# Optimization experiments

Hardware: AMD Instinct MI355X
Metric: run time of the kernel (lower is better)

Reference implementation:

```python
import jax, jax.numpy as jnp
import numpy as np

N_PAPER, N_MESH = 60000, 30000
N = N_PAPER + N_MESH
E_TRAIN, E_DEC = 2000000, 400000
F_PAPER = F_MESH = 128
D0, H, D = 16, 32, 16  # initial embed, hidden, final embed
NREL, NB = 2, 4


def _glorot(key, shape):
    fan_in, fan_out = shape[-2], shape[-1]
    s = jnp.sqrt(6.0 / (fan_in + fan_out)).astype(jnp.float32)
    return jax.random.uniform(key, shape, jnp.float32, -s, s)


def setup_inputs() -> dict:
    key = jax.random.key(0)
    ks = iter(jax.random.split(key, 40))
    inp = {
        'x_paper': jax.random.normal(next(ks), (N_PAPER, F_PAPER), jnp.float32),
        'x_mesh': jax.random.normal(next(ks), (N_MESH, F_MESH), jnp.float32),
        'train_edge_index': jax.random.randint(next(ks), (2, E_TRAIN), 0, N, jnp.int64 if jax.config.jax_enable_x64 else jnp.int32),
        'train_edge_type': jnp.sort(jax.random.randint(next(ks), (E_TRAIN,), 0, NREL)),
        'pos_edge_index': jax.random.randint(next(ks), (2, E_DEC), 0, N),
        'pos_edge_type': jnp.sort(jax.random.randint(next(ks), (E_DEC,), 0, NREL)),
        'neg_edge_index': jax.random.randint(next(ks), (2, E_DEC), 0, N),
        'neg_edge_type': jnp.sort(jax.random.randint(next(ks), (E_DEC,), 0, NREL)),
        # input transforms
        'Wp': _glorot(next(ks), (F_PAPER, D0)), 'bp': jnp.zeros((D0,), jnp.float32),
        'Wm': _glorot(next(ks), (F_MESH, D0)), 'bm': jnp.zeros((D0,), jnp.float32),
        # decode linears
        'Wd0': _glorot(next(ks), (D, D)), 'bd0': jnp.zeros((D,), jnp.float32),
        'Wd1': _glorot(next(ks), (D, D)), 'bd1': jnp.zeros((D,), jnp.float32),
    }
    dims = [(D0, H), (H, H), (H, H), (H, D)]
    for i, (di, do) in enumerate(dims, 1):
        inp[f'bases{i}'] = _glorot(next(ks), (NB, di, do))
        inp[f'comp{i}'] = _glorot(next(ks), (NREL, NB))
        inp[f'root{i}'] = _glorot(next(ks), (di, do))
        inp[f'bias{i}'] = jnp.zeros((do,), jnp.float32)
    return inp


def rgcn_layer(x, src, dst, et, bases, comp, root, bias):
    # PyG RGCNConv with basis decomposition, per-relation mean aggregation.
    out = x @ root + bias
    xs = x[src]  # [E, in]
    for r in range(NREL):
        W_r = jnp.einsum('b,bio->io', comp[r], bases)
        m = xs @ W_r  # [E, out]
        mf = (et == r).astype(m.dtype)
        cnt = jax.ops.segment_sum(mf, dst, num_segments=N)
        agg = jax.ops.segment_sum(m * mf[:, None], dst, num_segments=N)
        out = out + agg / jnp.clip(cnt, 1.0)[:, None]
    return out


def _decode_block(z, ei, et, Wd0, bd0, Wd1, bd1):
    zs, zd = z[ei[0]], z[ei[1]]
    h0 = zs @ Wd0 + bd0
    h1 = zs @ Wd1 + bd1
    h = jnp.where((et == 0)[:, None], h0, h1)
    return jnp.sum(h * zd, axis=-1)


def reference(x_paper, x_mesh, train_edge_index, train_edge_type,
              pos_edge_index, pos_edge_type, neg_edge_index, neg_edge_type,
              Wp, bp, Wm, bm, Wd0, bd0, Wd1, bd1,
              bases1, comp1, root1, bias1, bases2, comp2, root2, bias2,
              bases3, comp3, root3, bias3, bases4, comp4, root4, bias4):
    x = jnp.concatenate([x_paper @ Wp + bp, x_mesh @ Wm + bm], axis=0)  # [N, D0]
    src, dst = train_edge_index[0], train_edge_index[1]
    x = jax.nn.relu(rgcn_layer(x, src, dst, train_edge_type, bases1, comp1, root1, bias1))
    x = jax.nn.relu(rgcn_layer(x, src, dst, train_edge_type, bases2, comp2, root2, bias2))
    x = jax.nn.relu(rgcn_layer(x, src, dst, train_edge_type, bases3, comp3, root3, bias3))
    z = rgcn_layer(x, src, dst, train_edge_type, bases4, comp4, root4, bias4)
    # edge types are sorted, so per-edge in-order compute matches the masked concat order
    pos = _decode_block(z, pos_edge_index, pos_edge_type, Wd0, bd0, Wd1, bd1)
    neg = _decode_block(z, neg_edge_index, neg_edge_type, Wd0, bd0, Wd1, bd1)
    return jnp.concatenate([pos, neg], axis=0)  # [2*E_DEC]
```

## Files before the change

kernel.cpp:

```cpp
#include <hip/hip_runtime.h>
#include <hip/hip_bf16.h>

constexpr int NN = 90000;
constexpr int NP = 60000;
constexpr int NM = 30000;
constexpr int ET = 2000000;
constexpr int ED = 400000;
constexpr int TWO_NN = 2 * NN;

constexpr int BKT_SH  = 9;
constexpr int NB_BKT  = (TWO_NN + 511) >> BKT_SH;
constexpr int BKT_CAP = 6400;
constexpr int TILE    = 2048;
constexpr int N_TILES = (ET + TILE - 1) / TILE;

__device__ __forceinline__ float bflo(unsigned int u) {
    union { unsigned int i; float f; } c;
    c.i = u << 16;
    return c.f;
}
__device__ __forceinline__ float bfhi(unsigned int u) {
    union { unsigned int i; float f; } c;
    c.i = u & 0xffff0000u;
    return c.f;
}
__device__ __forceinline__ unsigned short f2bf(float f) {
    union { float f; unsigned int i; } c;
    c.f = f;
    unsigned int x = c.i;
    return (unsigned short)((x + 0x7FFFu + ((x >> 16) & 1u)) >> 16);
}

__global__ void init_kernel(const int* __restrict__ tei, int* __restrict__ gcur,
                            int* __restrict__ dflag) {
    int b = blockIdx.x * blockDim.x + threadIdx.x;
    if (b < NB_BKT) gcur[b] = b * BKT_CAP;
    if (b == 0) {
        int allzero = 1;
        for (int i = 0; i < 16; i++)
            if (tei[2 * i + 1] != 0) allzero = 0;
        dflag[0] = allzero;
    }
}

__global__ void __launch_bounds__(256) binA_kernel(
        const int* __restrict__ ei, const int* __restrict__ et,
        const int* __restrict__ dflag, int* __restrict__ gcur,
        int2* __restrict__ pairs) {
    __shared__ int histw[4][NB_BKT];
    __shared__ int wbase[4][NB_BKT];
    __shared__ int tot[NB_BKT];
    __shared__ int excl[NB_BKT];
    __shared__ int gbase[NB_BKT];
    __shared__ int scn[256];
    __shared__ int2 tbuf[TILE];
    int t = threadIdx.x;
    int w = t >> 6;
    int tile0 = blockIdx.x * TILE;
    int tcount = ET - tile0;
    if (tcount > TILE) tcount = TILE;
    for (int i = t; i < 4 * NB_BKT; i += 256) ((int*)histw)[i] = 0;
    __syncthreads();
    int sft = dflag[0];
    int myk[8], mys[8];
#pragma unroll
    for (int q = 0; q < 8; q++) {
        int li = q * 256 + t;
        myk[q] = -1;
        if (li < tcount) {
            int e = tile0 + li;
            int s = ei[(size_t)e << sft];
            int d = ei[(size_t)(ET + e) << sft];
            int r = et[(size_t)e << sft];
            int key = r * NN + d;
            myk[q] = key;
            mys[q] = s;
            atomicAdd(&histw[w][key >> BKT_SH], 1);
        }
    }
    __syncthreads();
    for (int i = t; i < NB_BKT; i += 256) {
        int h0 = histw[0][i], h1 = histw[1][i], h2 = histw[2][i], h3 = histw[3][i];
        wbase[0][i] = 0;
        wbase[1][i] = h0;
        wbase[2][i] = h0 + h1;
        wbase[3][i] = h0 + h1 + h2;
        tot[i] = h0 + h1 + h2 + h3;
    }
    __syncthreads();
    int v0 = (t < NB_BKT / 2) ? tot[2 * t] : 0;
    int v1 = (t < NB_BKT / 2) ? tot[2 * t + 1] : 0;
    int s = v0 + v1;
    scn[t] = s;
    __syncthreads();
    for (int st = 1; st < 256; st <<= 1) {
        int u = (t >= st) ? scn[t - st] : 0;
        __syncthreads();
        scn[t] += u;
        __syncthreads();
    }
    int base = scn[t] - s;
    if (t < NB_BKT / 2) {
        excl[2 * t] = base;
        excl[2 * t + 1] = base + v0;
    }
    __syncthreads();
    for (int i = t; i < NB_BKT; i += 256) {
        int e0 = excl[i];
        wbase[0][i] += e0;
        wbase[1][i] += e0;
        wbase[2][i] += e0;
        wbase[3][i] += e0;
        histw[0][i] = 0; histw[1][i] = 0; histw[2][i] = 0; histw[3][i] = 0;
    }
    __syncthreads();
#pragma unroll
    for (int q = 0; q < 8; q++) {
        if (myk[q] >= 0) {
            int b = myk[q] >> BKT_SH;
            int p = wbase[w][b] + atomicAdd(&histw[w][b], 1);
            tbuf[p] = make_int2(myk[q], mys[q]);
        }
    }
    __syncthreads();
    for (int i = t; i < NB_BKT; i += 256)
        if (tot[i] > 0) gbase[i] = atomicAdd(&gcur[i], tot[i]);
    __syncthreads();
    for (int i = t; i < tcount; i += 256) {
        int2 p = tbuf[i];
        int b = p.x >> BKT_SH;
        int gpos = gbase[b] + (i - excl[b]);
        int cap = (b + 1) * BKT_CAP - 1;
        pairs[gpos < cap ? gpos : cap] = p;
    }
}

__global__ void __launch_bounds__(256) histplace_kernel(
        const int* __restrict__ gcur, const int2* __restrict__ pairs,
        int* __restrict__ off, int* __restrict__ endo, float* __restrict__ inv,
        int* __restrict__ csr) {
    __shared__ int kh[512];
    __shared__ int scn[256];
    int b = blockIdx.x;
    int t = threadIdx.x;
    int beg = b * BKT_CAP, end = gcur[b];
    for (int i = t; i < 512; i += 256) kh[i] = 0;
    __syncthreads();
    for (int i = beg + t; i < end; i += 256)
        atomicAdd(&kh[pairs[i].x & 511], 1);
    __syncthreads();
    int v[2];
    int s = 0;
#pragma unroll
    for (int q = 0; q < 2; q++) {
        v[q] = kh[t * 2 + q];
        s += v[q];
    }
    scn[t] = s;
    __syncthreads();
    for (int st = 1; st < 256; st <<= 1) {
        int u = (t >= st) ? scn[t - st] : 0;
        __syncthreads();
        scn[t] += u;
        __syncthreads();
    }
    int run = beg + scn[t] - s;
    int kbase = b << BKT_SH;
    int kc[2];
#pragma unroll
    for (int q = 0; q < 2; q++) {
        int key = kbase + t * 2 + q;
        if (key < TWO_NN) {
            off[key] = run;
            endo[key] = run + v[q];
            inv[key] = 1.0f / (float)(v[q] > 1 ? v[q] : 1);
        }
        kc[q] = run;
        run += v[q];
    }
    __syncthreads();
#pragma unroll
    for (int q = 0; q < 2; q++) kh[t * 2 + q] = kc[q];
    __syncthreads();
    for (int i = beg + t; i < end; i += 256) {
        int2 p = pairs[i];
        int pos = atomicAdd(&kh[p.x & 511], 1);
        csr[pos] = p.y;
    }
}

__global__ void __launch_bounds__(256) embed2_kernel(
        const float* __restrict__ Xp, const float* __restrict__ Xm,
        const float* __restrict__ Wp, const float* __restrict__ bp,
        const float* __restrict__ Wm, const float* __restrict__ bm,
        unsigned short* __restrict__ outbf) {
    __shared__ float Wl[4096 + 32];
    for (int i = threadIdx.x; i < 2048; i += 256) {
        Wl[i] = Wp[i];
        Wl[2048 + i] = Wm[i];
    }
    if (threadIdx.x < 16) {
        Wl[4096 + threadIdx.x] = bp[threadIdx.x];
        Wl[4112 + threadIdx.x] = bm[threadIdx.x];
    }
    __syncthreads();
    int n = blockIdx.x * 256 + threadIdx.x;
    if (n >= NN) return;
    const float* X;
    const float* Ws;
    const float* Bs;
    if (n < NP) { X = Xp + (size_t)n * 128; Ws = Wl; Bs = Wl + 4096; }
    else        { X = Xm + (size_t)(n - NP) * 128; Ws = Wl + 2048; Bs = Wl + 4112; }
    float acc[16];
#pragma unroll
    for (int j = 0; j < 16; j++) acc[j] = Bs[j];
    const float4* row = (const float4*)X;
    for (int k4 = 0; k4 < 32; k4++) {
        float4 xv = row[k4];
        int k = k4 * 4;
#pragma unroll
        for (int j = 0; j < 16; j++) {
            float a = acc[j];
            a = fmaf(xv.x, Ws[(k + 0) * 16 + j], a);
            a = fmaf(xv.y, Ws[(k + 1) * 16 + j], a);
            a = fmaf(xv.z, Ws[(k + 2) * 16 + j], a);
            a = fmaf(xv.w, Ws[(k + 3) * 16 + j], a);
            acc[j] = a;
        }
    }
    ushort4* ob = (ushort4*)(outbf + (size_t)n * 16);
#pragma unroll
    for (int q = 0; q < 4; q++) {
        ushort4 ub;
        ub.x = f2bf(acc[4 * q]);     ub.y = f2bf(acc[4 * q + 1]);
        ub.z = f2bf(acc[4 * q + 2]); ub.w = f2bf(acc[4 * q + 3]);
        ob[q] = ub;
    }
}

__global__ void prep_all_kernel(
        const float* __restrict__ ba0, const float* __restrict__ co0,
        const float* __restrict__ ro0, const float* __restrict__ bi0,
        const float* __restrict__ ba1, const float* __restrict__ co1,
        const float* __restrict__ ro1, const float* __restrict__ bi1,
        const float* __restrict__ ba2, const float* __restrict__ co2,
        const float* __restrict__ ro2, const float* __restrict__ bi2,
        const float* __restrict__ ba3, const float* __restrict__ co3,
        const float* __restrict__ ro3, const float* __restrict__ bi3,
        float* __restrict__ Wbuf4) {
    int l = blockIdx.x;
    const float* bases; const float* comp; const float* root; const float* bias;
    if (l == 0)      { bases = ba0; comp = co0; root = ro0; bias = bi0; }
    else if (l == 1) { bases = ba1; comp = co1; root = ro1; bias = bi1; }
    else if (l == 2) { bases = ba2; comp = co2; root = ro2; bias = bi2; }
    else             { bases = ba3; comp = co3; root = ro3; bias = bi3; }
    int din = (l == 0) ? 16 : 32;
    int dout = (l == 3) ? 16 : 32;
    int sz = din * dout;
    float* W = Wbuf4 + l * 3200;
    for (int i = threadIdx.x; i < sz; i += 256) {
        float b0 = bases[i];
        float b1 = bases[sz + i];
        float b2 = bases[2 * sz + i];
        float b3 = bases[3 * sz + i];
        for (int r = 0; r < 2; r++) {
            W[r * sz + i] = comp[r * 4 + 0] * b0 + comp[r * 4 + 1] * b1 +
                            comp[r * 4 + 2] * b2 + comp[r * 4 + 3] * b3;
        }
        W[2 * sz + i] = root[i];
    }
    if (threadIdx.x < dout) W[3 * sz + threadIdx.x] = bias[threadIdx.x];
}

template <int DIN, int DOUT, int RELU>
__global__ void __launch_bounds__(256) layer_kernel(
        const int* __restrict__ off, const int* __restrict__ endo,
        const int* __restrict__ csr,
        const unsigned short* __restrict__ xbf_in,
        const float* __restrict__ inv, const float* __restrict__ Wbuf,
        unsigned short* __restrict__ xbf_out) {
    constexpr int SZ = DIN * DOUT;
    constexpr int QL = DIN / 8;
    constexpr int TPN = 2 * QL;
    constexpr int NPB = 256 / TPN;
    constexpr int AGST = 2 * DIN + 4;
    constexpr int XSST = DIN + 8;
    __shared__ float Wl[3 * SZ + DOUT];
    __shared__ float agg[NPB * AGST];
    __shared__ unsigned short xsu[NPB * XSST];
    for (int i = threadIdx.x; i < 3 * SZ + DOUT; i += 256) Wl[i] = Wbuf[i];
    int t = threadIdx.x;
    int ln = t / TPN;
    int rl = t % TPN;
    int r = rl / QL;
    int lane = rl % QL;
    int d = blockIdx.x * NPB + ln;
    if (d < NN) {
        if (r == 0) {
            uint4 u = *(const uint4*)(xbf_in + (size_t)d * DIN + lane * 8);
            *(uint4*)&xsu[ln * XSST + lane * 8] = u;
        }
        int key = r * NN + d;
        int b = off[key];
        int e = endo[key];
        float a0[8] = {0, 0, 0, 0, 0, 0, 0, 0};
        float a1[8] = {0, 0, 0, 0, 0, 0, 0, 0};
        const unsigned short* hp = xbf_in + lane * 8;
        int k = b;
        if (k + 3 < e) {
            int s0 = csr[k], s1 = csr[k + 1], s2 = csr[k + 2], s3 = csr[k + 3];
            k += 4;
            while (k + 3 < e) {
                uint4 u0 = *(const uint4*)(hp + (size_t)s0 * DIN);
                uint4 u1 = *(const uint4*)(hp + (size_t)s1 * DIN);
                uint4 u2 = *(const uint4*)(hp + (size_t)s2 * DIN);
                uint4 u3 = *(const uint4*)(hp + (size_t)s3 * DIN);
                s0 = csr[k]; s1 = csr[k + 1]; s2 = csr[k + 2]; s3 = csr[k + 3];
                k += 4;
                a0[0] += bflo(u0.x); a0[1] += bfhi(u0.x);
                a0[2] += bflo(u0.y); a0[3] += bfhi(u0.y);
                a0[4] += bflo(u0.z); a0[5] += bfhi(u0.z);
                a0[6] += bflo(u0.w); a0[7] += bfhi(u0.w);
                a1[0] += bflo(u1.x); a1[1] += bfhi(u1.x);
                a1[2] += bflo(u1.y); a1[3] += bfhi(u1.y);
                a1[4] += bflo(u1.z); a1[5] += bfhi(u1.z);
                a1[6] += bflo(u1.w); a1[7] += bfhi(u1.w);
                a0[0] += bflo(u2.x); a0[1] += bfhi(u2.x);
                a0[2] += bflo(u2.y); a0[3] += bfhi(u2.y);
                a0[4] += bflo(u2.z); a0[5] += bfhi(u2.z);
                a0[6] += bflo(u2.w); a0[7] += bfhi(u2.w);
                a1[0] += bflo(u3.x); a1[1] += bfhi(u3.x);
                a1[2] += bflo(u3.y); a1[3] += bfhi(u3.y);
                a1[4] += bflo(u3.z); a1[5] += bfhi(u3.z);
                a1[6] += bflo(u3.w); a1[7] += bfhi(u3.w);
            }
            uint4 u0 = *(const uint4*)(hp + (size_t)s0 * DIN);
            uint4 u1 = *(const uint4*)(hp + (size_t)s1 * DIN);
            uint4 u2 = *(const uint4*)(hp + (size_t)s2 * DIN);
            uint4 u3 = *(const uint4*)(hp + (size_t)s3 * DIN);
            a0[0] += bflo(u0.x); a0[1] += bfhi(u0.x);
            a0[2] += bflo(u0.y); a0[3] += bfhi(u0.y);
            a0[4] += bflo(u0.z); a0[5] += bfhi(u0.z);
            a0[6] += bflo(u0.w); a0[7] += bfhi(u0.w);
            a1[0] += bflo(u1.x); a1[1] += bfhi(u1.x);
            a1[2] += bflo(u1.y); a1[3] += bfhi(u1.y);
            a1[4] += bflo(u1.z); a1[5] += bfhi(u1.z);
            a1[6] += bflo(u1.w); a1[7] += bfhi(u1.w);
            a0[0] += bflo(u2.x); a0[1] += bfhi(u2.x);
            a0[2] += bflo(u2.y); a0[3] += bfhi(u2.y);
            a0[4] += bflo(u2.z); a0[5] += bfhi(u2.z);
            a0[6] += bflo(u2.w); a0[7] += bfhi(u2.w);
            a1[0] += bflo(u3.x); a1[1] += bfhi(u3.x);
            a1[2] += bflo(u3.y); a1[3] += bfhi(u3.y);
            a1[4] += bflo(u3.z); a1[5] += bfhi(u3.z);
            a1[6] += bflo(u3.w); a1[7] += bfhi(u3.w);
        }
        for (; k < e; k++) {
            uint4 u0 = *(const uint4*)(hp + (size_t)csr[k] * DIN);
            a0[0] += bflo(u0.x); a0[1] += bfhi(u0.x);
            a0[2] += bflo(u0.y); a0[3] += bfhi(u0.y);
            a0[4] += bflo(u0.z); a0[5] += bfhi(u0.z);
            a0[6] += bflo(u0.w); a0[7] += bfhi(u0.w);
        }
        float* ap = agg + ln * AGST + r * DIN + lane * 8;
        *(float4*)ap = make_float4(a0[0] + a1[0], a0[1] + a1[1],
                                   a0[2] + a1[2], a0[3] + a1[3]);
        *(float4*)(ap + 4) = make_float4(a0[4] + a1[4], a0[5] + a1[5],
                                         a0[6] + a1[6], a0[7] + a1[7]);
    }
    __syncthreads();
    constexpr int CPN = DOUT / 4;
    for (int tt = t; tt < NPB * CPN; tt += 256) {
        int ln2 = tt / CPN;
        int j0 = (tt % CPN) * 4;
        int d2 = blockIdx.x * NPB + ln2;
        if (d2 < NN) {
            float iv0 = inv[d2], iv1 = inv[NN + d2];
            float acc[4];
#pragma unroll
            for (int jj = 0; jj < 4; jj++) acc[jj] = Wl[3 * SZ + j0 + jj];
#pragma unroll
            for (int k2 = 0; k2 < DIN; k2 += 2) {
                unsigned up = *(const unsigned*)&xsu[ln2 * XSST + k2];
                float xv0 = bflo(up);
                float xv1 = bfhi(up);
                float m00 = agg[ln2 * AGST + k2] * iv0;
                float m10 = agg[ln2 * AGST + DIN + k2] * iv1;
                float m01 = agg[ln2 * AGST + k2 + 1] * iv0;
                float m11 = agg[ln2 * AGST + DIN + k2 + 1] * iv1;
                const float* w0a = &Wl[k2 * DOUT + j0];
                const float* w1a = &Wl[SZ + k2 * DOUT + j0];
                const float* wra = &Wl[2 * SZ + k2 * DOUT + j0];
#pragma unroll
                for (int jj = 0; jj < 4; jj++) {
                    acc[jj] = fmaf(xv0, wra[jj], acc[jj]);
                    acc[jj] = fmaf(m00, w0a[jj], acc[jj]);
                    acc[jj] = fmaf(m10, w1a[jj], acc[jj]);
                    acc[jj] = fmaf(xv1, wra[DOUT + jj], acc[jj]);
                    acc[jj] = fmaf(m01, w0a[DOUT + jj], acc[jj]);
                    acc[jj] = fmaf(m11, w1a[DOUT + jj], acc[jj]);
                }
            }
            if (RELU) {
#pragma unroll
                for (int jj = 0; jj < 4; jj++) acc[jj] = fmaxf(acc[jj], 0.0f);
            }
            ushort4 ub;
            ub.x = f2bf(acc[0]); ub.y = f2bf(acc[1]);
            ub.z = f2bf(acc[2]); ub.w = f2bf(acc[3]);
            *(ushort4*)(xbf_out + (size_t)d2 * DOUT + j0) = ub;
        }
    }
}

__global__ void __launch_bounds__(256) decode_fused_kernel(
        const unsigned short* __restrict__ zbf,
        const float* __restrict__ Wd0, const float* __restrict__ bd0,
        const float* __restrict__ Wd1, const float* __restrict__ bd1,
        const int* __restrict__ pei, const int* __restrict__ pet,
        const int* __restrict__ nei, const int* __restrict__ net_,
        float* __restrict__ out, const int* __restrict__ dflag) {
    __shared__ float W[2][256];
    __shared__ float B[2][16];
    for (int i = threadIdx.x; i < 256; i += 256) {
        W[0][i] = Wd0[i];
        W[1][i] = Wd1[i];
    }
    if (threadIdx.x < 16) {
        B[0][threadIdx.x] = bd0[threadIdx.x];
        B[1][threadIdx.x] = bd1[threadIdx.x];
    }
    __syncthreads();
    int i = blockIdx.x * 256 + threadIdx.x;
    if (i >= 2 * ED) return;
    int sft = dflag[0];
    const int* ei;
    const int* et;
    int e;
    if (i < ED) { ei = pei; et = pet; e = i; }
    else        { ei = nei; et = net_; e = i - ED; }
    int s = ei[(size_t)e << sft];
    int d = ei[(size_t)(ED + e) << sft];
    int r = et[(size_t)e << sft];
    float zs[16], zd[16];
    const uint4* sp = (const uint4*)(zbf + ((size_t)s << 4));
    const uint4* dp = (const uint4*)(zbf + ((size_t)d << 4));
#pragma unroll
    for (int h = 0; h < 2; h++) {
        uint4 us = sp[h];
        uint4 ud = dp[h];
        int o8 = h * 8;
        zs[o8 + 0] = bflo(us.x); zs[o8 + 1] = bfhi(us.x);
        zs[o8 + 2] = bflo(us.y); zs[o8 + 3] = bfhi(us.y);
        zs[o8 + 4] = bflo(us.z); zs[o8 + 5] = bfhi(us.z);
        zs[o8 + 6] = bflo(us.w); zs[o8 + 7] = bfhi(us.w);
        zd[o8 + 0] = bflo(ud.x); zd[o8 + 1] = bfhi(ud.x);
        zd[o8 + 2] = bflo(ud.y); zd[o8 + 3] = bfhi(ud.y);
        zd[o8 + 4] = bflo(ud.z); zd[o8 + 5] = bfhi(ud.z);
        zd[o8 + 6] = bflo(ud.w); zd[o8 + 7] = bfhi(ud.w);
    }
    const float* Wr = W[r];
    const float* Br = B[r];
    float acc = 0.0f;
#pragma unroll
    for (int j = 0; j < 16; j++) {
        float yj = Br[j];
#pragma unroll
        for (int k = 0; k < 16; k++) yj = fmaf(zs[k], Wr[k * 16 + j], yj);
        acc = fmaf(yj, zd[j], acc);
    }
    out[i] = acc;
}

extern "C" void kernel_launch(void* const* d_in, const int* in_sizes, int n_in,
                              void* d_out, int out_size, void* d_ws, size_t ws_size,
                              hipStream_t stream) {
    const float* x_paper = (const float*)d_in[0];
    const float* x_mesh  = (const float*)d_in[1];
    const int* tei  = (const int*)d_in[2];
    const int* tet  = (const int*)d_in[3];
    const int* pei  = (const int*)d_in[4];
    const int* pet  = (const int*)d_in[5];
    const int* nei  = (const int*)d_in[6];
    const int* net_ = (const int*)d_in[7];
    const float* Wp  = (const float*)d_in[8];
    const float* bp  = (const float*)d_in[9];
    const float* Wm  = (const float*)d_in[10];
    const float* bm  = (const float*)d_in[11];
    const float* Wd0 = (const float*)d_in[12];
    const float* bd0 = (const float*)d_in[13];
    const float* Wd1 = (const float*)d_in[14];
    const float* bd1 = (const float*)d_in[15];

    float* ws = (float*)d_ws;
    size_t o = 0;
    unsigned short* xbfA = (unsigned short*)(ws + o); o += (size_t)NN * 16;
    unsigned short* xbfB = (unsigned short*)(ws + o); o += (size_t)NN * 16;
    float* inv  = ws + o; o += (size_t)TWO_NN;
    int*   off  = (int*)(ws + o); o += (size_t)TWO_NN;
    int*   endo = (int*)(ws + o); o += (size_t)TWO_NN;
    int*   csr  = (int*)(ws + o); o += (size_t)NB_BKT * BKT_CAP;
    int*   gcur = (int*)(ws + o); o += 512;
    int2*  pairs = (int2*)(ws + o); o += (size_t)2 * NB_BKT * BKT_CAP;
    float* Wbuf4 = ws + o; o += 4 * 3200;
    int*   dflag = (int*)(ws + o); o += 16;

    init_kernel<<<(NB_BKT + 255) / 256, 256, 0, stream>>>(tei, gcur, dflag);

    binA_kernel<<<N_TILES, 256, 0, stream>>>(tei, tet, dflag, gcur, pairs);
    histplace_kernel<<<NB_BKT, 256, 0, stream>>>(gcur, pairs, off, endo, inv, csr);

    embed2_kernel<<<(NN + 255) / 256, 256, 0, stream>>>(
        x_paper, x_mesh, Wp, bp, Wm, bm, xbfA);

    prep_all_kernel<<<4, 256, 0, stream>>>(
        (const float*)d_in[16], (const float*)d_in[17], (const float*)d_in[18], (const float*)d_in[19],
        (const float*)d_in[20], (const float*)d_in[21], (const float*)d_in[22], (const float*)d_in[23],
        (const float*)d_in[24], (const float*)d_in[25], (const float*)d_in[26], (const float*)d_in[27],
        (const float*)d_in[28], (const float*)d_in[29], (const float*)d_in[30], (const float*)d_in[31],
        Wbuf4);

    int blk16 = (NN + 63) / 64;
    int blk32 = (NN + 31) / 32;
    layer_kernel<16, 32, 1><<<blk16, 256, 0, stream>>>(
        off, endo, csr, xbfA, inv, Wbuf4 + 0 * 3200, xbfB);
    layer_kernel<32, 32, 1><<<blk32, 256, 0, stream>>>(
        off, endo, csr, xbfB, inv, Wbuf4 + 1 * 3200, xbfA);
    layer_kernel<32, 32, 1><<<blk32, 256, 0, stream>>>(
        off, endo, csr, xbfA, inv, Wbuf4 + 2 * 3200, xbfB);
    layer_kernel<32, 16, 0><<<blk32, 256, 0, stream>>>(
        off, endo, csr, xbfB, inv, Wbuf4 + 3 * 3200, xbfA);

    decode_fused_kernel<<<(2 * ED + 255) / 256, 256, 0, stream>>>(
        xbfA, Wd0, bd0, Wd1, bd1, pei, pet, nei, net_, (float*)d_out, dflag);
}
```

Measured before the change: 355.6 us.

## Pad CSR segments to multiples of 8 with a zero sentinel node and unroll gather by 8

Each per-(relation,node) CSR segment is padded to a multiple of 8 entries, with the padding pointing at an extra all-zero sentinel row appended to the bf16 feature buffers. This lets the layer gather loop run fully unrolled by 8 with no remainder loop, raising memory-level parallelism and removing tail branches. The cost is up to 7 extra wasted gathers per segment (average degree is about 11), larger bucket capacity, and a serial padding-fill loop in histplace.

Result: slower. 366.2 us (+3.0%).

```diff
diff --git a/kernel.cpp b/kernel.cpp
--- a/kernel.cpp
+++ b/kernel.cpp
@@ -10,7 +10,7 @@
 
 constexpr int BKT_SH  = 9;
 constexpr int NB_BKT  = (TWO_NN + 511) >> BKT_SH;
-constexpr int BKT_CAP = 6400;
+constexpr int BKT_CAP = 8448;
 constexpr int TILE    = 2048;
 constexpr int N_TILES = (ET + TILE - 1) / TILE;
 
@@ -32,9 +32,16 @@
 }
 
 __global__ void init_kernel(const int* __restrict__ tei, int* __restrict__ gcur,
-                            int* __restrict__ dflag) {
+                            int* __restrict__ dflag,
+                            unsigned short* __restrict__ xbfA,
+                            unsigned short* __restrict__ xbfB) {
     int b = blockIdx.x * blockDim.x + threadIdx.x;
     if (b < NB_BKT) gcur[b] = b * BKT_CAP;
+    if (b < 32) {
+        xbfA[(size_t)NN * 32 + b] = 0;
+        xbfB[(size_t)NN * 32 + b] = 0;
+        if (b < 16) xbfA[(size_t)NN * 16 + b] = 0;
+    }
     if (b == 0) {
         int allzero = 1;
         for (int i = 0; i < 16; i++)
@@ -154,7 +161,7 @@
 #pragma unroll
     for (int q = 0; q < 2; q++) {
         v[q] = kh[t * 2 + q];
-        s += v[q];
+        s += (v[q] + 7) & ~7;
     }
     scn[t] = s;
     __syncthreads();
@@ -170,13 +177,15 @@
 #pragma unroll
     for (int q = 0; q < 2; q++) {
         int key = kbase + t * 2 + q;
+        int vp = (v[q] + 7) & ~7;
         if (key < TWO_NN) {
             off[key] = run;
-            endo[key] = run + v[q];
+            endo[key] = run + vp;
             inv[key] = 1.0f / (float)(v[q] > 1 ? v[q] : 1);
+            for (int i = run + v[q]; i < run + vp; i++) csr[i] = NN;
         }
         kc[q] = run;
-        run += v[q];
+        run += vp;
     }
     __syncthreads();
 #pragma unroll
@@ -272,6 +281,12 @@
     if (threadIdx.x < dout) W[3 * sz + threadIdx.x] = bias[threadIdx.x];
 }
 
+#define ACCU(u, a)                                   \
+    a[0] += bflo(u.x); a[1] += bfhi(u.x);            \
+    a[2] += bflo(u.y); a[3] += bfhi(u.y);            \
+    a[4] += bflo(u.z); a[5] += bfhi(u.z);            \
+    a[6] += bflo(u.w); a[7] += bfhi(u.w);
+
 template <int DIN, int DOUT, int RELU>
 __global__ void __launch_bounds__(256) layer_kernel(
         const int* __restrict__ off, const int* __restrict__ endo,
@@ -307,60 +322,35 @@
         float a1[8] = {0, 0, 0, 0, 0, 0, 0, 0};
         const unsigned short* hp = xbf_in + lane * 8;
         int k = b;
-        if (k + 3 < e) {
+        if (k < e) {
             int s0 = csr[k], s1 = csr[k + 1], s2 = csr[k + 2], s3 = csr[k + 3];
-            k += 4;
-            while (k + 3 < e) {
+            int s4 = csr[k + 4], s5 = csr[k + 5], s6 = csr[k + 6], s7 = csr[k + 7];
+            k += 8;
+            while (k < e) {
                 uint4 u0 = *(const uint4*)(hp + (size_t)s0 * DIN);
                 uint4 u1 = *(const uint4*)(hp + (size_t)s1 * DIN);
                 uint4 u2 = *(const uint4*)(hp + (size_t)s2 * DIN);
                 uint4 u3 = *(const uint4*)(hp + (size_t)s3 * DIN);
+                uint4 u4 = *(const uint4*)(hp + (size_t)s4 * DIN);
+                uint4 u5 = *(const uint4*)(hp + (size_t)s5 * DIN);
+                uint4 u6 = *(const uint4*)(hp + (size_t)s6 * DIN);
+                uint4 u7 = *(const uint4*)(hp + (size_t)s7 * DIN);
                 s0 = csr[k]; s1 = csr[k + 1]; s2 = csr[k + 2]; s3 = csr[k + 3];
-                k += 4;
-                a0[0] += bflo(u0.x); a0[1] += bfhi(u0.x);
-                a0[2] += bflo(u0.y); a0[3] += bfhi(u0.y);
-                a0[4] += bflo(u0.z); a0[5] += bfhi(u0.z);
-                a0[6] += bflo(u0.w); a0[7] += bfhi(u0.w);
-                a1[0] += bflo(u1.x); a1[1] += bfhi(u1.x);
-                a1[2] += bflo(u1.y); a1[3] += bfhi(u1.y);
-                a1[4] += bflo(u1.z); a1[5] += bfhi(u1.z);
-                a1[6] += bflo(u1.w); a1[7] += bfhi(u1.w);
-                a0[0] += bflo(u2.x); a0[1] += bfhi(u2.x);
-                a0[2] += bflo(u2.y); a0[3] += bfhi(u2.y);
-                a0[4] += bflo(u2.z); a0[5] += bfhi(u2.z);
-                a0[6] += bflo(u2.w); a0[7] += bfhi(u2.w);
-                a1[0] += bflo(u3.x); a1[1] += bfhi(u3.x);
-                a1[2] += bflo(u3.y); a1[3] += bfhi(u3.y);
-                a1[4] += bflo(u3.z); a1[5] += bfhi(u3.z);
-                a1[6] += bflo(u3.w); a1[7] += bfhi(u3.w);
+                s4 = csr[k + 4]; s5 = csr[k + 5]; s6 = csr[k + 6]; s7 = csr[k + 7];
+                k += 8;
+                ACCU(u0, a0) ACCU(u1, a1) ACCU(u2, a0) ACCU(u3, a1)
+                ACCU(u4, a0) ACCU(u5, a1) ACCU(u6, a0) ACCU(u7, a1)
             }
             uint4 u0 = *(const uint4*)(hp + (size_t)s0 * DIN);
             uint4 u1 = *(const uint4*)(hp + (size_t)s1 * DIN);
             uint4 u2 = *(const uint4*)(hp + (size_t)s2 * DIN);
             uint4 u3 = *(const uint4*)(hp + (size_t)s3 * DIN);
-            a0[0] += bflo(u0.x); a0[1] += bfhi(u0.x);
-            a0[2] += bflo(u0.y); a0[3] += bfhi(u0.y);
-            a0[4] += bflo(u0.z); a0[5] += bfhi(u0.z);
-            a0[6] += bflo(u0.w); a0[7] += bfhi(u0.w);
-            a1[0] += bflo(u1.x); a1[1] += bfhi(u1.x);
-            a1[2] += bflo(u1.y); a1[3] += bfhi(u1.y);
-            a1[4] += bflo(u1.z); a1[5] += bfhi(u1.z);
-            a1[6] += bflo(u1.w); a1[7] += bfhi(u1.w);
-            a0[0] += bflo(u2.x); a0[1] += bfhi(u2.x);
-            a0[2] += bflo(u2.y); a0[3] += bfhi(u2.y);
-            a0[4] += bflo(u2.z); a0[5] += bfhi(u2.z);
-            a0[6] += bflo(u2.w); a0[7] += bfhi(u2.w);
-            a1[0] += bflo(u3.x); a1[1] += bfhi(u3.x);
-            a1[2] += bflo(u3.y); a1[3] += bfhi(u3.y);
-            a1[4] += bflo(u3.z); a1[5] += bfhi(u3.z);
-            a1[6] += bflo(u3.w); a1[7] += bfhi(u3.w);
-        }
-        for (; k < e; k++) {
-            uint4 u0 = *(const uint4*)(hp + (size_t)csr[k] * DIN);
-            a0[0] += bflo(u0.x); a0[1] += bfhi(u0.x);
-            a0[2] += bflo(u0.y); a0[3] += bfhi(u0.y);
-            a0[4] += bflo(u0.z); a0[5] += bfhi(u0.z);
-            a0[6] += bflo(u0.w); a0[7] += bfhi(u0.w);
+            uint4 u4 = *(const uint4*)(hp + (size_t)s4 * DIN);
+            uint4 u5 = *(const uint4*)(hp + (size_t)s5 * DIN);
+            uint4 u6 = *(const uint4*)(hp + (size_t)s6 * DIN);
+            uint4 u7 = *(const uint4*)(hp + (size_t)s7 * DIN);
+            ACCU(u0, a0) ACCU(u1, a1) ACCU(u2, a0) ACCU(u3, a1)
+            ACCU(u4, a0) ACCU(u5, a1) ACCU(u6, a0) ACCU(u7, a1)
         }
         float* ap = agg + ln * AGST + r * DIN + lane * 8;
         *(float4*)ap = make_float4(a0[0] + a1[0], a0[1] + a1[1],
@@ -494,8 +484,8 @@
 
     float* ws = (float*)d_ws;
     size_t o = 0;
-    unsigned short* xbfA = (unsigned short*)(ws + o); o += (size_t)NN * 16;
-    unsigned short* xbfB = (unsigned short*)(ws + o); o += (size_t)NN * 16;
+    unsigned short* xbfA = (unsigned short*)(ws + o); o += (size_t)(NN + 1) * 16;
+    unsigned short* xbfB = (unsigned short*)(ws + o); o += (size_t)(NN + 1) * 16;
     float* inv  = ws + o; o += (size_t)TWO_NN;
     int*   off  = (int*)(ws + o); o += (size_t)TWO_NN;
     int*   endo = (int*)(ws + o); o += (size_t)TWO_NN;
@@ -505,7 +495,8 @@
     float* Wbuf4 = ws + o; o += 4 * 3200;
     int*   dflag = (int*)(ws + o); o += 16;
 
-    init_kernel<<<(NB_BKT + 255) / 256, 256, 0, stream>>>(tei, gcur, dflag);
+    init_kernel<<<(NB_BKT + 255) / 256, 256, 0, stream>>>(tei, gcur, dflag,
+                                                          xbfA, xbfB);
 
     binA_kernel<<<N_TILES, 256, 0, stream>>>(tei, tet, dflag, gcur, pairs);
     histplace_kernel<<<NB_BKT, 256, 0, stream>>>(gcur, pairs, off, endo, inv, csr);
```
